# Performance work log

Hardware: AMD Instinct MI355X
Metric: run time of the kernel (lower is better)

Reference implementation:

```python
import jax, jax.numpy as jnp
import numpy as np
from jax import lax

B_, L_, D_MODEL = 2, 2048, 1024
H, P, N, G, K, CHUNK = 32, 64, 128, 1, 4, 256
INTER = H * P                 # 2048
CONV_DIM = INTER + 2 * G * N  # 2304
PROJ = INTER + CONV_DIM + H   # 4384: [gate | hidden_B_C | dt]
EPS = 1e-6


def segment_sum(x):
    # x: [..., T] -> [..., T, T]; segsum[i,j] = sum_{k=j+1..i} x[k] for i>=j, else -inf
    T = x.shape[-1]
    xx = jnp.repeat(x[..., None], T, axis=-1)
    xx = jnp.where(jnp.tril(jnp.ones((T, T), bool), -1), xx, 0.0)
    s = jnp.cumsum(xx, axis=-2)
    return jnp.where(jnp.tril(jnp.ones((T, T), bool)), s, -jnp.inf)


def setup_inputs() -> dict:
    key = jax.random.key(0)
    ks = jax.random.split(key, 6)
    s = 0.02
    return {
        "x": jax.random.normal(ks[0], (B_, L_, D_MODEL), jnp.float32),
        "in_proj_w": jax.random.normal(ks[1], (PROJ, D_MODEL), jnp.float32) * s,
        "conv_w": jax.random.normal(ks[2], (CONV_DIM, 1, K), jnp.float32) * s,
        "conv_b": jnp.zeros((CONV_DIM,), jnp.float32),
        "dt_bias": jax.random.uniform(ks[3], (H,), jnp.float32, 0.0, 1.0),
        "A_log": jnp.log(jnp.arange(1, H + 1, dtype=jnp.float32)),
        "D": jnp.ones((H,), jnp.float32),
        "norm_w": jnp.ones((INTER,), jnp.float32),
        "out_proj_w": jax.random.normal(ks[4], (D_MODEL, INTER), jnp.float32) * s,
    }


def _forward(x, in_proj_w, conv_w, conv_b, dt_bias, A_log, D, norm_w, out_proj_w):
    b, L, _ = x.shape
    proj = x @ in_proj_w.T                                    # [b,L,PROJ]
    gate, hBC, dt = jnp.split(proj, [INTER, INTER + CONV_DIM], axis=-1)
    # depthwise causal conv1d over sequence
    xc = jnp.pad(hBC.transpose(0, 2, 1), ((0, 0), (0, 0), (K - 1, 0)))
    conv = lax.conv_general_dilated(xc, conv_w, (1,), 'VALID',
                                    dimension_numbers=('NCH', 'OIH', 'NCH'),
                                    feature_group_count=CONV_DIM)
    hBC = jax.nn.silu((conv + conv_b[None, :, None]).transpose(0, 2, 1))  # [b,L,CONV_DIM]
    hs, Bm, Cm = jnp.split(hBC, [INTER, INTER + G * N], axis=-1)
    hs = hs.reshape(b, L, H, P)
    Bm = jnp.repeat(Bm.reshape(b, L, G, N), H // G, axis=2)   # [b,L,H,N]
    Cm = jnp.repeat(Cm.reshape(b, L, G, N), H // G, axis=2)
    dt = jax.nn.softplus(dt + dt_bias)                        # [b,L,H]
    A = -jnp.exp(A_log)                                       # [H]
    D_res = hs * D[None, None, :, None]
    hs = hs * dt[..., None]
    Adt = dt * A                                              # [b,L,H]
    c = L // CHUNK
    A_c = Adt.reshape(b, c, CHUNK, H).transpose(0, 3, 1, 2)   # [b,H,c,l]
    A_cum = jnp.cumsum(A_c, axis=-1)
    Lmat = jnp.exp(segment_sum(A_c))                          # [b,H,c,l,l]
    hs_c = hs.reshape(b, c, CHUNK, H, P)
    B_c = Bm.reshape(b, c, CHUNK, H, N)
    C_c = Cm.reshape(b, c, CHUNK, H, N)
    # intra-chunk (diagonal blocks)
    Gm = jnp.einsum('bcshn,bczhn->bchsz', C_c, B_c)
    M = Gm * Lmat.transpose(0, 2, 1, 3, 4)
    Y_diag = jnp.einsum('bchsz,bczhp->bcshp', M, hs_c)
    # per-chunk final states
    decay_states = jnp.exp(A_cum[..., -1:] - A_cum)           # [b,H,c,l]
    B_decay = B_c * decay_states.transpose(0, 2, 3, 1)[..., None]
    states = jnp.einsum('bclhn,bclhp->bchpn', B_decay, hs_c)  # [b,c,H,P,N]
    # inter-chunk recurrence
    decay_chunk = jnp.exp(segment_sum(jnp.pad(A_cum[..., -1], ((0, 0), (0, 0), (1, 0)))))  # [b,H,c+1,c+1]
    states0 = jnp.concatenate([jnp.zeros_like(states[:, :1]), states], axis=1)             # [b,c+1,H,P,N]
    prev = jnp.einsum('bhij,bjhpn->bihpn', decay_chunk, states0)[:, :-1]                   # [b,c,H,P,N]
    # off-diagonal contribution
    state_decay = jnp.exp(A_cum).transpose(0, 2, 3, 1)        # [b,c,l,H]
    Y_off = jnp.einsum('bclhn,bchpn->bclhp', C_c, prev) * state_decay[..., None]
    y = ((Y_diag + Y_off).reshape(b, L, H, P) + D_res).reshape(b, L, INTER)
    # gated grouped RMSNorm (group_size = INTER // G)
    gs = INTER // G
    yf = y.astype(jnp.float32) * jax.nn.silu(gate.astype(jnp.float32))
    yg = yf.reshape(b, L, INTER // gs, gs)
    var = jnp.mean(yg * yg, axis=-1, keepdims=True)
    yn = (yg * lax.rsqrt(var + EPS)).reshape(b, L, INTER) * norm_w
    return yn @ out_proj_w.T


def reference(x, in_proj_w, conv_w, conv_b, dt_bias, A_log, D, norm_w, out_proj_w):
    return _forward(x, in_proj_w, conv_w, conv_b, dt_bias, A_log, D, norm_w, out_proj_w)
```

## Files before the change

kernel.cpp:

```cpp
#include <hip/hip_runtime.h>
#include <stdint.h>

typedef __attribute__((ext_vector_type(8))) short short8;
typedef __attribute__((ext_vector_type(4))) float f32x4;

#define DEV static __device__ __forceinline__

DEV float b2f(unsigned short u) { union { float f; unsigned int i; } x; x.i = ((unsigned int)u) << 16; return x.f; }
DEV unsigned short f2b(float f) {
    union { float f; unsigned int i; } x; x.f = f;
    unsigned int r = x.i + 0x7fffu + ((x.i >> 16) & 1u);
    return (unsigned short)(r >> 16);
}
DEV void gld_lds16(const void* g, void* l) {
    __builtin_amdgcn_global_load_lds((const __attribute__((address_space(1))) void*)g,
                                     (__attribute__((address_space(3))) void*)l, 16, 0, 0);
}
DEV int xcd_swizzle(int bid, int nwg) {
    int q = nwg >> 3, r = nwg & 7;
    int xcd = bid & 7, base = bid >> 3;
    return (xcd < r ? xcd * (q + 1) : r * (q + 1) + (xcd - r) * q) + base;
}

__global__ void cast3_kernel(const float* __restrict__ a, unsigned short* __restrict__ oa, long na8,
                             const float* __restrict__ b, unsigned short* __restrict__ ob_, long nb8,
                             const float* __restrict__ c, unsigned short* __restrict__ oc, long nc8) {
    long i = (long)blockIdx.x * blockDim.x + threadIdx.x;
    long stride = (long)gridDim.x * blockDim.x;
    long tot = na8 + nb8 + nc8;
    for (; i < tot; i += stride) {
        const float* src; unsigned short* dst; long j = i;
        if (j < na8) { src = a; dst = oa; }
        else if (j < na8 + nb8) { j -= na8; src = b; dst = ob_; }
        else { j -= na8 + nb8; src = c; dst = oc; }
        const f32x4* p = (const f32x4*)(src + j * 8);
        f32x4 v0 = p[0], v1 = p[1];
        short8 o;
        o[0] = (short)f2b(v0[0]); o[1] = (short)f2b(v0[1]); o[2] = (short)f2b(v0[2]); o[3] = (short)f2b(v0[3]);
        o[4] = (short)f2b(v1[0]); o[5] = (short)f2b(v1[1]); o[6] = (short)f2b(v1[2]); o[7] = (short)f2b(v1[3]);
        *(short8*)(dst + j * 8) = o;
    }
}

template<int OMODE>
__global__ __launch_bounds__(256) void gemm_nt(
    const unsigned short* __restrict__ A, int lda, long sAy, long sAz,
    const unsigned short* __restrict__ B, int ldb, long sBy, long sBz,
    void* __restrict__ Cp, int ldc, long sCy, long sCz,
    float* __restrict__ aux,
    int M, int N, int K, int tn)
{
    A += (long)blockIdx.y * sAy + (long)blockIdx.z * sAz;
    B += (long)blockIdx.y * sBy + (long)blockIdx.z * sBz;
    int bid = xcd_swizzle(blockIdx.x, gridDim.x);
    int im = bid / tn, in_ = bid % tn;
    int m0 = im * 128, n0 = in_ * 128;
    __shared__ short smem[2 * 2 * 128 * 64];
    int tid = threadIdx.x;
    int lane = tid & 63, wave = tid >> 6;
    int wu = __builtin_amdgcn_readfirstlane(wave);
    int wm = wave >> 1, wn = wave & 1;
    f32x4 acc[4][4];
#pragma unroll
    for (int m = 0; m < 4; m++)
#pragma unroll
        for (int n = 0; n < 4; n++) acc[m][n] = (f32x4){0.f, 0.f, 0.f, 0.f};

    auto stage = [&](int k0, int s) {
        short* As = smem + s * 16384;
        short* Bs = As + 8192;
#pragma unroll
        for (int i = 0; i < 4; ++i) {
            int g = i * 256 + tid;
            int r = g >> 3, pc = g & 7;
            int cc = pc ^ (r & 7);
            gld_lds16(A + (long)(m0 + r) * lda + k0 + cc * 8, As + (i * 256 + wu * 64) * 8);
            int rb = n0 + r; rb = rb < N ? rb : N - 1;
            gld_lds16(B + (long)rb * ldb + k0 + cc * 8, Bs + (i * 256 + wu * 64) * 8);
        }
    };

    int nt = K >> 6;
    stage(0, 0);
    for (int t = 0; t < nt; ++t) {
        int cur = t & 1;
        if (t + 1 < nt) {
            stage((t + 1) << 6, cur ^ 1);
            asm volatile("s_waitcnt vmcnt(8)" ::: "memory");
        } else {
            asm volatile("s_waitcnt vmcnt(0)" ::: "memory");
        }
        __builtin_amdgcn_s_barrier();
        const short* As = smem + cur * 16384;
        const short* Bs = As + 8192;
#pragma unroll
        for (int ks = 0; ks < 2; ++ks) {
            short8 af[4], bfr[4];
#pragma unroll
            for (int m = 0; m < 4; ++m) {
                int r = wm * 64 + m * 16 + (lane & 15);
                int pc = (ks * 4 + (lane >> 4)) ^ (r & 7);
                af[m] = *(const short8*)(As + r * 64 + pc * 8);
            }
#pragma unroll
            for (int n = 0; n < 4; ++n) {
                int r = wn * 64 + n * 16 + (lane & 15);
                int pc = (ks * 4 + (lane >> 4)) ^ (r & 7);
                bfr[n] = *(const short8*)(Bs + r * 64 + pc * 8);
            }
            __builtin_amdgcn_s_setprio(1);
#pragma unroll
            for (int m = 0; m < 4; ++m)
#pragma unroll
                for (int n = 0; n < 4; ++n)
                    acc[m][n] = __builtin_amdgcn_mfma_f32_16x16x32_bf16(af[m], bfr[n], acc[m][n], 0, 0, 0);
            __builtin_amdgcn_s_setprio(0);
        }
        __builtin_amdgcn_s_barrier();
    }

    int rbase = m0 + wm * 64 + ((lane >> 4) << 2);
    int cbase = n0 + wn * 64 + (lane & 15);
    if (OMODE == 0) {
        float* C = (float*)Cp;
        C += (long)blockIdx.y * sCy + (long)blockIdx.z * sCz;
#pragma unroll
        for (int m = 0; m < 4; ++m)
#pragma unroll
            for (int n = 0; n < 4; ++n) {
                int col = cbase + n * 16;
                if (col < N) {
#pragma unroll
                    for (int r = 0; r < 4; ++r)
                        C[(long)(rbase + m * 16 + r) * ldc + col] = acc[m][n][r];
                }
            }
    } else if (OMODE == 4) {
        float* C = (float*)Cp;
#pragma unroll
        for (int m = 0; m < 4; ++m)
#pragma unroll
            for (int r = 0; r < 4; ++r) {
                int row = rbase + m * 16 + r;
                float sc = rsqrtf(aux[row] * (1.f / 2048.f) + 1e-6f);
#pragma unroll
                for (int n = 0; n < 4; ++n)
                    C[(long)row * ldc + cbase + n * 16] = acc[m][n][r] * sc;
            }
    } else {
        if (OMODE == 3) {
#pragma unroll
            for (int m = 0; m < 4; ++m)
#pragma unroll
                for (int n = 0; n < 4; ++n) {
                    int col = cbase + n * 16;
                    if (col >= 4352 && col < N) {
#pragma unroll
                        for (int r = 0; r < 4; ++r)
                            aux[(long)(rbase + m * 16 + r) * 32 + (col - 4352)] = acc[m][n][r];
                    }
                }
        }
        unsigned short* Cs = (unsigned short*)smem;
        int rl = wm * 64 + ((lane >> 4) << 2);
        int cl = wn * 64 + (lane & 15);
#pragma unroll
        for (int m = 0; m < 4; ++m)
#pragma unroll
            for (int r = 0; r < 4; ++r) {
                int row = rl + m * 16 + r;
                int xr = ((row >> 2) & 3) << 4;
#pragma unroll
                for (int n = 0; n < 4; ++n)
                    Cs[row * 128 + ((cl + n * 16) ^ xr)] = f2b(acc[m][n][r]);
            }
        __syncthreads();
        unsigned short* C = (unsigned short*)Cp;
        if (OMODE == 1) {
            C += (long)blockIdx.y * sCy + (long)blockIdx.z * sCz;
#pragma unroll
            for (int j = 0; j < 8; ++j) {
                int chunk = j * 256 + tid;
                int row = chunk >> 4, c8 = (chunk & 15) * 8;
                int col = n0 + c8;
                int xr = ((row >> 2) & 3) << 4;
                if (col < N)
                    *(short8*)(C + (long)(m0 + row) * ldc + col) = *(const short8*)(Cs + row * 128 + (c8 ^ xr));
            }
        } else {
#pragma unroll
            for (int j = 0; j < 8; ++j) {
                int idx = j * 256 + tid;
                int orr = idx >> 4, mc8 = (idx & 15) * 8;
                int ch = n0 + orr;
                if (ch < N) {
                    short8 o;
#pragma unroll
                    for (int q = 0; q < 8; ++q) {
                        int m = mc8 + q;
                        int xr = ((m >> 2) & 3) << 4;
                        o[q] = (short)Cs[m * 128 + (orr ^ xr)];
                    }
                    *(short8*)(C + (long)ch * ldc + m0 + mc8) = o;
                }
            }
        }
    }
}

__global__ __launch_bounds__(256) void dtcum_kernel(
    const float* __restrict__ dtraw,
    const float* __restrict__ dt_bias, const float* __restrict__ A_log,
    float* __restrict__ dtv, float* __restrict__ Acum, float* __restrict__ Atot)
{
    int bh = blockIdx.x;
    int b = bh >> 5, h = bh & 31;
    int tid = threadIdx.x;
    float bias = dt_bias[h];
    float negA = -__expf(A_log[h]);
    __shared__ float s[256];
    for (int c = 0; c < 8; ++c) {
        int t = c * 256 + tid;
        float v = dtraw[(long)(b * 2048 + t) * 32 + h] + bias;
        float dt = v > 20.f ? v : log1pf(__expf(v));
        dtv[(long)bh * 2048 + t] = dt;
        s[tid] = dt * negA;
        __syncthreads();
        for (int off = 1; off < 256; off <<= 1) {
            float x = (tid >= off) ? s[tid - off] : 0.f;
            __syncthreads();
            s[tid] += x;
            __syncthreads();
        }
        Acum[(long)bh * 2048 + t] = s[tid];
        if (tid == 255) Atot[bh * 8 + c] = s[255];
        __syncthreads();
    }
}

__global__ __launch_bounds__(256) void convT_kernel(
    const unsigned short* __restrict__ projT,
    const float* __restrict__ conv_w, const float* __restrict__ conv_b,
    const float* __restrict__ dtv, const float* __restrict__ Acum, const float* __restrict__ Atot,
    unsigned short* __restrict__ xdtT, unsigned short* __restrict__ xdtd,
    unsigned short* __restrict__ Bb, unsigned short* __restrict__ Cb, unsigned short* __restrict__ BT)
{
    int tt = blockIdx.x;
    int cht = blockIdx.y;
    int b = blockIdx.z;
    int t0 = tt * 256;
    int ch0 = cht * 64;
    int tid = threadIdx.x;
    __shared__ short raw[64 * 264];
    __shared__ unsigned short trsp[256 * 64];
    __shared__ float sdt[256], sac[256];
    __shared__ float satot;
    bool hidden = cht < 32;
    for (int j = 0; j < 9; ++j) {
        int idx = j * 256 + tid;
        if (idx < 64 * 33) {
            int r = idx / 33, cc = idx % 33;
            int tg = t0 - 8 + cc * 8;
            short8 v = {0, 0, 0, 0, 0, 0, 0, 0};
            if (tg >= 0)
                v = *(const short8*)(projT + (long)(2048 + ch0 + r) * 4096 + b * 2048 + tg);
            *(short8*)(raw + r * 264 + cc * 8) = v;
        }
    }
    if (hidden) {
        int h = cht;
        sdt[tid] = dtv[(long)(b * 32 + h) * 2048 + t0 + tid];
        sac[tid] = Acum[(long)(b * 32 + h) * 2048 + t0 + tid];
        if (tid == 0) satot = Atot[(b * 32 + h) * 8 + tt];
    }
    __syncthreads();
    for (int p = 0; p < 8; ++p) {
        int ch = p * 8 + (tid >> 5);
        int tb = (tid & 31) * 8;
        int cg = ch0 + ch;
        f32x4 wv = *(const f32x4*)(conv_w + cg * 4);
        float cb = conv_b[cg];
        float s[8];
#pragma unroll
        for (int j = 0; j < 8; ++j) {
            int tl = tb + j;
            float a = cb;
#pragma unroll
            for (int k = 0; k < 4; ++k)
                a += b2f((unsigned short)raw[ch * 264 + tl + 5 + k]) * wv[k];
            s[j] = a / (1.f + __expf(-a));
        }
        if (hidden) {
            short8 o1, o2;
#pragma unroll
            for (int j = 0; j < 8; ++j) {
                int tl = tb + j;
                float xdt = s[j] * sdt[tl];
                float dec = __expf(satot - sac[tl]);
                o1[j] = (short)f2b(xdt);
                o2[j] = (short)f2b(xdt * dec);
            }
            long off = (long)cg * 4096 + b * 2048 + t0 + tb;
            *(short8*)(xdtT + off) = o1;
            *(short8*)(xdtd + off) = o2;
        } else {
            short8 o;
#pragma unroll
            for (int j = 0; j < 8; ++j) o[j] = (short)f2b(s[j]);
            if (cht < 34) {
                int n = (cht - 32) * 64 + ch;
                *(short8*)(BT + (long)n * 4096 + b * 2048 + t0 + tb) = o;
            }
#pragma unroll
            for (int j = 0; j < 8; ++j) {
                int tl = tb + j;
                trsp[tl * 64 + (ch ^ ((tl & 7) << 3))] = (unsigned short)o[j];
            }
        }
    }
    if (!hidden) {
        __syncthreads();
        unsigned short* dst = (cht < 34) ? Bb : Cb;
        int n0 = ((cht - 32) & 1) * 64;
        for (int p = 0; p < 8; ++p) {
            int idx = p * 256 + tid;
            int tl = idx >> 3, c8 = (idx & 7) * 8;
            short8 o;
#pragma unroll
            for (int q = 0; q < 8; ++q)
                o[q] = (short)trsp[tl * 64 + ((c8 + q) ^ ((tl & 7) << 3))];
            *(short8*)(dst + (long)(b * 2048 + t0 + tl) * 128 + n0 + c8) = o;
        }
    }
}

__global__ __launch_bounds__(256) void ydiagoff_kernel(
    const unsigned short* __restrict__ Gm,
    const float* __restrict__ Acum,
    const unsigned short* __restrict__ xdtT,
    const unsigned short* __restrict__ projT,
    const unsigned short* __restrict__ Cb,
    const unsigned short* __restrict__ prevb,
    const float* __restrict__ dtv,
    const float* __restrict__ Dp,
    const float* __restrict__ norm_w,
    unsigned short* __restrict__ ynu,
    float* __restrict__ ssq)
{
    int blk = blockIdx.x;
    int h = blk & 31, bc = blk >> 5;
    int c = bc & 7, b = bc >> 3;
    int tid = threadIdx.x, lane = tid & 63, wave = tid >> 6;
    __shared__ float sAc[256];
    __shared__ short Mb[256 * 64];
    __shared__ float sdt[256];
    sAc[tid] = Acum[(long)(b * 32 + h) * 2048 + c * 256 + tid];
    __syncthreads();
    f32x4 acc[4][4];
#pragma unroll
    for (int m = 0; m < 4; m++)
#pragma unroll
        for (int n = 0; n < 4; n++) acc[m][n] = (f32x4){0.f, 0.f, 0.f, 0.f};

    for (int zp = 0; zp < 4; ++zp) {
#pragma unroll
        for (int i = 0; i < 8; ++i) {
            int ci = i * 256 + tid;
            int s = ci >> 3, cz = ci & 7;
            int z0 = zp * 64 + cz * 8;
            short8 gv = *(const short8*)(Gm + ((long)bc * 256 + s) * 256 + z0);
            float as = sAc[s];
            short8 o;
#pragma unroll
            for (int j = 0; j < 8; ++j) {
                int z = z0 + j;
                float e = (s >= z) ? __expf(as - sAc[z]) : 0.f;
                o[j] = (short)f2b(b2f((unsigned short)gv[j]) * e);
            }
            *(short8*)(Mb + s * 64 + (cz ^ (s & 7)) * 8) = o;
        }
        __syncthreads();
#pragma unroll
        for (int ks = 0; ks < 2; ++ks) {
            short8 af[4], bfr[4];
#pragma unroll
            for (int m = 0; m < 4; ++m) {
                int r = wave * 64 + m * 16 + (lane & 15);
                int pc = (ks * 4 + (lane >> 4)) ^ (r & 7);
                af[m] = *(const short8*)(Mb + r * 64 + pc * 8);
            }
#pragma unroll
            for (int n = 0; n < 4; ++n) {
                int p = n * 16 + (lane & 15);
                int zcol = c * 256 + zp * 64 + ks * 32 + (lane >> 4) * 8;
                bfr[n] = *(const short8*)(xdtT + (long)(h * 64 + p) * 4096 + b * 2048 + zcol);
            }
#pragma unroll
            for (int m = 0; m < 4; ++m)
#pragma unroll
                for (int n = 0; n < 4; ++n)
                    acc[m][n] = __builtin_amdgcn_mfma_f32_16x16x32_bf16(af[m], bfr[n], acc[m][n], 0, 0, 0);
        }
        __syncthreads();
    }
    float el[4];
#pragma unroll
    for (int m = 0; m < 4; ++m) el[m] = __expf(sAc[wave * 64 + m * 16 + (lane & 15)]);
#pragma unroll
    for (int ks = 0; ks < 4; ++ks) {
        short8 af[4], bfr[4];
#pragma unroll
        for (int m = 0; m < 4; ++m) {
            int l = wave * 64 + m * 16 + (lane & 15);
            short8 cv = *(const short8*)(Cb + ((long)b * 2048 + c * 256 + l) * 128 + ks * 32 + (lane >> 4) * 8);
#pragma unroll
            for (int j = 0; j < 8; ++j) af[m][j] = (short)f2b(b2f((unsigned short)cv[j]) * el[m]);
        }
#pragma unroll
        for (int n = 0; n < 4; ++n) {
            int p = n * 16 + (lane & 15);
            bfr[n] = *(const short8*)(prevb + ((long)(bc * 32 + h) * 64 + p) * 128 + ks * 32 + (lane >> 4) * 8);
        }
#pragma unroll
        for (int m = 0; m < 4; ++m)
#pragma unroll
            for (int n = 0; n < 4; ++n)
                acc[m][n] = __builtin_amdgcn_mfma_f32_16x16x32_bf16(af[m], bfr[n], acc[m][n], 0, 0, 0);
    }
    unsigned short* gt = (unsigned short*)Mb;
#pragma unroll
    for (int i = 0; i < 8; ++i) {
        int idx = i * 256 + tid;
        int r = idx >> 5, c8 = (idx & 31) * 8;
        short8 v = *(const short8*)(projT + (long)(h * 64 + r) * 4096 + b * 2048 + c * 256 + c8);
#pragma unroll
        for (int j = 0; j < 8; ++j)
            gt[r * 256 + ((c8 + j) ^ ((r & 7) << 3))] = (unsigned short)v[j];
    }
    sdt[tid] = dtv[(long)(b * 32 + h) * 2048 + c * 256 + tid];
    __syncthreads();
    float Dv = Dp[h];
#pragma unroll
    for (int m = 0; m < 4; ++m)
#pragma unroll
        for (int r = 0; r < 4; ++r) {
            int tl = wave * 64 + m * 16 + ((lane >> 4) << 2) + r;
            long bt = (long)b * 2048 + c * 256 + tl;
            float part = 0.f;
#pragma unroll
            for (int n = 0; n < 4; ++n) {
                int cl = n * 16 + (lane & 15);
                int ch = h * 64 + cl;
                float xv = b2f(xdtT[(long)ch * 4096 + bt]);
                float yv = acc[m][n][r] + (xv / sdt[tl]) * Dv;
                float g = b2f(gt[cl * 256 + (tl ^ ((cl & 7) << 3))]);
                float yf = yv * g / (1.f + __expf(-g));
                part += yf * yf;
                ynu[bt * 2048 + ch] = f2b(yf * norm_w[ch]);
            }
#pragma unroll
            for (int w2 = 1; w2 < 16; w2 <<= 1) part += __shfl_xor(part, w2);
            if ((lane & 15) == 0) atomicAdd(&ssq[bt], part);
        }
}

__global__ __launch_bounds__(256) void scan_kernel(
    const float* __restrict__ states,
    const float* __restrict__ Atot,
    unsigned short* __restrict__ prevb)
{
    int bh = blockIdx.x;
    int b = bh >> 5, h = bh & 31;
    float ex[8];
#pragma unroll
    for (int c = 0; c < 8; ++c) ex[c] = __expf(Atot[bh * 8 + c]);
    for (int e = threadIdx.x; e < 8192; e += 256) {
        float S = 0.f;
#pragma unroll
        for (int c = 0; c < 8; ++c) {
            long idx = (long)((b * 8 + c) * 32 + h) * 8192 + e;
            prevb[idx] = f2b(S);
            S = ex[c] * S + states[idx];
        }
    }
}

extern "C" void kernel_launch(void* const* d_in, const int* in_sizes, int n_in,
                              void* d_out, int out_size, void* d_ws, size_t ws_size,
                              hipStream_t stream)
{
    const float* x        = (const float*)d_in[0];
    const float* in_proj  = (const float*)d_in[1];
    const float* conv_w   = (const float*)d_in[2];
    const float* conv_b   = (const float*)d_in[3];
    const float* dt_bias  = (const float*)d_in[4];
    const float* A_log    = (const float*)d_in[5];
    const float* Dp       = (const float*)d_in[6];
    const float* norm_w   = (const float*)d_in[7];
    const float* out_proj = (const float*)d_in[8];
    float* out = (float*)d_out;

    char* w = (char*)d_ws;
    auto alloc = [&](size_t bytes) { char* p = w; w += (bytes + 255) & ~(size_t)255; return p; };
    unsigned short* xb    = (unsigned short*)alloc(4096L * 1024 * 2);
    unsigned short* wb    = (unsigned short*)alloc(4384L * 1024 * 2);
    unsigned short* ob    = (unsigned short*)alloc(1024L * 2048 * 2);
    unsigned short* projT = (unsigned short*)alloc(4384L * 4096 * 2);
    float*          dtraw = (float*)        alloc(4096L * 32 * 4);
    float*          dtv   = (float*)        alloc(64L * 2048 * 4);
    float*          Acum  = (float*)        alloc(64L * 2048 * 4);
    float*          Atot  = (float*)        alloc(64L * 8 * 4);
    unsigned short* xdtT  = (unsigned short*)alloc(2048L * 4096 * 2);
    unsigned short* xdtd  = (unsigned short*)alloc(2048L * 4096 * 2);
    unsigned short* Bb    = (unsigned short*)alloc(4096L * 128 * 2);
    unsigned short* Cb    = (unsigned short*)alloc(4096L * 128 * 2);
    unsigned short* BT    = (unsigned short*)alloc(128L * 4096 * 2);
    unsigned short* Gmb   = (unsigned short*)alloc(16L * 256 * 256 * 2);
    float*          states= (float*)        alloc(2L * 8 * 2048 * 128 * 4);
    unsigned short* prevb = (unsigned short*)alloc(2L * 8 * 2048 * 128 * 2);
    unsigned short* ynu   = (unsigned short*)alloc(4096L * 2048 * 2);
    float*          ssq   = (float*)        alloc(4096L * 4);

    hipMemsetAsync(ssq, 0, 4096 * 4, stream);

    cast3_kernel<<<2048, 256, 0, stream>>>(x, xb, 4096L * 1024 / 8,
                                           in_proj, wb, 4384L * 1024 / 8,
                                           out_proj, ob, 1024L * 2048 / 8);

    gemm_nt<3><<<dim3(32 * 35, 1, 1), 256, 0, stream>>>(
        xb, 1024, 0, 0, wb, 1024, 0, 0, projT, 4096, 0, 0, dtraw, 4096, 4384, 1024, 35);

    dtcum_kernel<<<64, 256, 0, stream>>>(dtraw, dt_bias, A_log, dtv, Acum, Atot);

    convT_kernel<<<dim3(8, 36, 2), 256, 0, stream>>>(
        projT, conv_w, conv_b, dtv, Acum, Atot, xdtT, xdtd, Bb, Cb, BT);

    gemm_nt<1><<<dim3(4, 8, 2), 256, 0, stream>>>(
        Cb, 128, 256L * 128, 2048L * 128,
        Bb, 128, 256L * 128, 2048L * 128,
        Gmb, 256, 256L * 256, 8L * 256 * 256, nullptr, 256, 256, 128, 2);

    gemm_nt<0><<<dim3(16, 8, 2), 256, 0, stream>>>(
        xdtd, 4096, 256, 2048,
        BT, 4096, 256, 2048,
        states, 128, 2048L * 128, 8L * 2048 * 128, nullptr, 2048, 128, 256, 1);

    scan_kernel<<<64, 256, 0, stream>>>(states, Atot, prevb);

    ydiagoff_kernel<<<512, 256, 0, stream>>>(Gmb, Acum, xdtT, projT, Cb, prevb,
                                             dtv, Dp, norm_w, ynu, ssq);

    gemm_nt<4><<<dim3(32 * 8, 1, 1), 256, 0, stream>>>(
        ynu, 2048, 0, 0, ob, 2048, 0, 0, out, 1024, 0, 0, ssq, 4096, 1024, 2048, 8);
}
```

Measured before the change: 305.6 us.

## Fold D residual into intra-chunk matrix diagonal and vectorize transposed GEMM epilogue

The D*x skip term is folded into the diagonal of the decay-weighted intra-chunk matrix as D/dt, since the right-hand operand is x*dt. This removes the per-element strided global gather of xdtT and the division in the output epilogue. The transposed-output GEMM epilogue now stages its tile in LDS in transposed, swizzled form, so each thread reads a contiguous short8 instead of eight scalar LDS reads. The diagonal term is rounded to bf16 together with the G value, which slightly changes numerics.

```diff
diff --git a/kernel.cpp b/kernel.cpp
--- a/kernel.cpp
+++ b/kernel.cpp
@@ -147,6 +147,32 @@
                 for (int n = 0; n < 4; ++n)
                     C[(long)row * ldc + cbase + n * 16] = acc[m][n][r] * sc;
             }
+    } else if (OMODE == 1) {
+        unsigned short* Cs = (unsigned short*)smem;
+        int rl = wm * 64 + ((lane >> 4) << 2);
+        int cl = wn * 64 + (lane & 15);
+#pragma unroll
+        for (int m = 0; m < 4; ++m)
+#pragma unroll
+            for (int r = 0; r < 4; ++r) {
+                int row = rl + m * 16 + r;
+                int xr = ((row >> 2) & 3) << 4;
+#pragma unroll
+                for (int n = 0; n < 4; ++n)
+                    Cs[row * 128 + ((cl + n * 16) ^ xr)] = f2b(acc[m][n][r]);
+            }
+        __syncthreads();
+        unsigned short* C = (unsigned short*)Cp;
+        C += (long)blockIdx.y * sCy + (long)blockIdx.z * sCz;
+#pragma unroll
+        for (int j = 0; j < 8; ++j) {
+            int chunk = j * 256 + tid;
+            int row = chunk >> 4, c8 = (chunk & 15) * 8;
+            int col = n0 + c8;
+            int xr = ((row >> 2) & 3) << 4;
+            if (col < N)
+                *(short8*)(C + (long)(m0 + row) * ldc + col) = *(const short8*)(Cs + row * 128 + (c8 ^ xr));
+        }
     } else {
         if (OMODE == 3) {
 #pragma unroll
@@ -161,48 +187,31 @@
                     }
                 }
         }
-        unsigned short* Cs = (unsigned short*)smem;
+        unsigned short* T = (unsigned short*)smem;
         int rl = wm * 64 + ((lane >> 4) << 2);
         int cl = wn * 64 + (lane & 15);
 #pragma unroll
-        for (int m = 0; m < 4; ++m)
-#pragma unroll
-            for (int r = 0; r < 4; ++r) {
-                int row = rl + m * 16 + r;
-                int xr = ((row >> 2) & 3) << 4;
-#pragma unroll
-                for (int n = 0; n < 4; ++n)
-                    Cs[row * 128 + ((cl + n * 16) ^ xr)] = f2b(acc[m][n][r]);
-            }
+        for (int n = 0; n < 4; ++n) {
+            int ch = cl + n * 16;
+            int sw = (ch & 15) << 3;
+#pragma unroll
+            for (int m = 0; m < 4; ++m)
+#pragma unroll
+                for (int r = 0; r < 4; ++r) {
+                    int mrow = rl + m * 16 + r;
+                    T[ch * 128 + (mrow ^ sw)] = f2b(acc[m][n][r]);
+                }
+        }
         __syncthreads();
         unsigned short* C = (unsigned short*)Cp;
-        if (OMODE == 1) {
-            C += (long)blockIdx.y * sCy + (long)blockIdx.z * sCz;
-#pragma unroll
-            for (int j = 0; j < 8; ++j) {
-                int chunk = j * 256 + tid;
-                int row = chunk >> 4, c8 = (chunk & 15) * 8;
-                int col = n0 + c8;
-                int xr = ((row >> 2) & 3) << 4;
-                if (col < N)
-                    *(short8*)(C + (long)(m0 + row) * ldc + col) = *(const short8*)(Cs + row * 128 + (c8 ^ xr));
-            }
-        } else {
-#pragma unroll
-            for (int j = 0; j < 8; ++j) {
-                int idx = j * 256 + tid;
-                int orr = idx >> 4, mc8 = (idx & 15) * 8;
-                int ch = n0 + orr;
-                if (ch < N) {
-                    short8 o;
-#pragma unroll
-                    for (int q = 0; q < 8; ++q) {
-                        int m = mc8 + q;
-                        int xr = ((m >> 2) & 3) << 4;
-                        o[q] = (short)Cs[m * 128 + (orr ^ xr)];
-                    }
-                    *(short8*)(C + (long)ch * ldc + m0 + mc8) = o;
-                }
+#pragma unroll
+        for (int j = 0; j < 8; ++j) {
+            int idx = j * 256 + tid;
+            int ch = idx >> 4, mc8 = (idx & 15) * 8;
+            int gch = n0 + ch;
+            if (gch < N) {
+                short8 o = *(const short8*)(T + ch * 128 + (mc8 ^ ((ch & 15) << 3)));
+                *(short8*)(C + (long)gch * ldc + m0 + mc8) = o;
             }
         }
     }
@@ -353,8 +362,10 @@
     int tid = threadIdx.x, lane = tid & 63, wave = tid >> 6;
     __shared__ float sAc[256];
     __shared__ short Mb[256 * 64];
-    __shared__ float sdt[256];
+    __shared__ float sdi[256];
+    float Dv = Dp[h];
     sAc[tid] = Acum[(long)(b * 32 + h) * 2048 + c * 256 + tid];
+    sdi[tid] = Dv / dtv[(long)(b * 32 + h) * 2048 + c * 256 + tid];
     __syncthreads();
     f32x4 acc[4][4];
 #pragma unroll
@@ -375,7 +386,9 @@
             for (int j = 0; j < 8; ++j) {
                 int z = z0 + j;
                 float e = (s >= z) ? __expf(as - sAc[z]) : 0.f;
-                o[j] = (short)f2b(b2f((unsigned short)gv[j]) * e);
+                float mval = b2f((unsigned short)gv[j]) * e;
+                if (s == z) mval += sdi[s];
+                o[j] = (short)f2b(mval);
             }
             *(short8*)(Mb + s * 64 + (cz ^ (s & 7)) * 8) = o;
         }
@@ -437,9 +450,7 @@
         for (int j = 0; j < 8; ++j)
             gt[r * 256 + ((c8 + j) ^ ((r & 7) << 3))] = (unsigned short)v[j];
     }
-    sdt[tid] = dtv[(long)(b * 32 + h) * 2048 + c * 256 + tid];
     __syncthreads();
-    float Dv = Dp[h];
 #pragma unroll
     for (int m = 0; m < 4; ++m)
 #pragma unroll
@@ -451,8 +462,7 @@
             for (int n = 0; n < 4; ++n) {
                 int cl = n * 16 + (lane & 15);
                 int ch = h * 64 + cl;
-                float xv = b2f(xdtT[(long)ch * 4096 + bt]);
-                float yv = acc[m][n][r] + (xv / sdt[tl]) * Dv;
+                float yv = acc[m][n][r];
                 float g = b2f(gt[cl * 256 + (tl ^ ((cl & 7) << 3))]);
                 float yf = yv * g / (1.f + __expf(-g));
                 part += yf * yf;
```

After: 311.9 us. +2.1%, slower.
